# Kernel tuning notes

Measured on AMD Instinct MI355X. Metric: run time of the kernel, lower is better.

Reference implementation:

```python
import jax, jax.numpy as jnp
import numpy as np

V, D, H, L, B, S = 32000, 512, 512, 2, 64, 64
PAD = 0
NEG = -1000000000.0


def setup_inputs() -> dict:
    key = jax.random.key(0)
    ks = jax.random.split(key, 12)
    s = 0.05
    X = jax.random.randint(ks[0], (B, S), 0, V)
    enc = jax.random.normal(ks[1], (B, S - 1, H), jnp.float32)
    mask = jnp.zeros((S - 1, S - 1), dtype=bool)
    emb = jax.random.normal(ks[2], (V, D), jnp.float32) * s
    lstm_Wih = jax.random.normal(ks[3], (L, 4 * H, D), jnp.float32) * s  # D == H so stacking works for layer>0
    lstm_Whh = jax.random.normal(ks[4], (L, 4 * H, H), jnp.float32) * s
    lstm_bih = jax.random.normal(ks[5], (L, 4 * H), jnp.float32) * s
    lstm_bhh = jax.random.normal(ks[6], (L, 4 * H), jnp.float32) * s
    attn_Wh = jax.random.normal(ks[7], (H, H), jnp.float32) * s  # attn weight cols acting on decoder hidden
    attn_We = jax.random.normal(ks[8], (H, H), jnp.float32) * s  # attn weight cols acting on encoder outputs
    attn_b = jax.random.normal(ks[9], (H,), jnp.float32) * s
    v_w = jax.random.normal(ks[10], (H,), jnp.float32) * s
    fc_W = jax.random.normal(ks[11], (V, 2 * H), jnp.float32) * s
    fc_b = jnp.zeros((V,), jnp.float32)
    return {"X": X, "encoderOutputs": enc, "mask": mask, "emb": emb,
            "lstm_Wih": lstm_Wih, "lstm_Whh": lstm_Whh, "lstm_bih": lstm_bih, "lstm_bhh": lstm_bhh,
            "attn_Wh": attn_Wh, "attn_We": attn_We, "attn_b": attn_b, "v_w": v_w,
            "fc_W": fc_W, "fc_b": fc_b}


def _forward(X, enc, mask, emb, Wih, Whh, bih, bhh, attn_Wh, attn_We, attn_b, v_w, fc_W, fc_b):
    Bn, Sn = X.shape
    T = Sn - 1
    E = emb[X[:, :-1]]  # [B,T,D]
    # encoder part of attention projection is time-invariant: hoist out of the loop
    enc_proj = jnp.einsum('beh,kh->bek', enc, attn_We) + attn_b  # [B,T,H]
    h0 = jnp.zeros((L, Bn, H), E.dtype)
    c0 = jnp.zeros((L, Bn, H), E.dtype)
    xs = (jnp.transpose(E, (1, 0, 2)), X[:, 1:].T, jnp.arange(T))

    def step(carry, x_t):
        h, c = carry
        e_t, tgt, t = x_t
        inp = e_t
        hs, cs = [], []
        for l in range(L):  # fixed small layer loop
            g = inp @ Wih[l].T + h[l] @ Whh[l].T + bih[l] + bhh[l]
            i, f, gg, o = jnp.split(g, 4, axis=-1)  # torch gate order i,f,g,o
            cn = jax.nn.sigmoid(f) * c[l] + jax.nn.sigmoid(i) * jnp.tanh(gg)
            hn = jax.nn.sigmoid(o) * jnp.tanh(cn)
            hs.append(hn); cs.append(cn)
            inp = hn
        h = jnp.stack(hs); c = jnp.stack(cs)
        top = inp  # [B,H] == LSTM output of last layer
        energy = jnp.tanh((top @ attn_Wh.T)[:, None, :] + enc_proj)  # [B,T,H]
        scores = energy @ v_w  # [B,T]
        # original: self.mask[t-1] (python negative wrap) then mask.unsqueeze(0).unsqueeze(1)
        m = mask[(t - 1) % mask.shape[0], :T]  # [T]
        s3 = jnp.where(m[None, None, :], NEG, scores[None])  # broadcast -> [1,B,T]
        att = jax.nn.softmax(s3, axis=1)[0]  # softmax over batch dim, as in original
        weighted = jnp.einsum('be,beh->bh', att, enc)
        logits = jnp.concatenate([top, weighted], axis=1) @ fc_W.T + fc_b  # [B,V]
        logp = jax.nn.log_softmax(logits, axis=-1)
        nll = -jnp.take_along_axis(logp, tgt[:, None], axis=1)[:, 0]
        valid = tgt != PAD
        loss_t = jnp.sum(jnp.where(valid, nll, 0.0)) / jnp.sum(valid)  # CE mean with ignore_index
        return (h, c), loss_t

    _, losses = jax.lax.scan(step, (h0, c0), xs)
    return jnp.mean(losses)  # totalLoss / (seq_len - 1)


def reference(X, encoderOutputs, mask, emb, lstm_Wih, lstm_Whh, lstm_bih, lstm_bhh, attn_Wh, attn_We, attn_b, v_w, fc_W, fc_b):
    return _forward(X, encoderOutputs, mask, emb, lstm_Wih, lstm_Whh, lstm_bih, lstm_bhh, attn_Wh, attn_We, attn_b, v_w, fc_W, fc_b)
```

## Files before the change

### kernel.cpp

```cpp
#include <hip/hip_runtime.h>
#include <math.h>

#define NEGV -1000000000.0f

typedef unsigned short u16;
typedef __attribute__((ext_vector_type(8))) short bf16x8;
typedef __attribute__((ext_vector_type(4))) float f32x4;

__device__ __forceinline__ u16 f2bf(float f){
  union { float f; unsigned u; } v; v.f = f;
  unsigned u = v.u;
  unsigned r = (u + 0x7fffu + ((u >> 16) & 1u)) >> 16;
  return (u16)r;
}
__device__ __forceinline__ float bf2f(u16 b){
  union { unsigned u; float f; } v; v.u = ((unsigned)b) << 16;
  return v.f;
}
__device__ __forceinline__ float sigmf(float x){ return 1.f / (1.f + __expf(-x)); }
__device__ __forceinline__ float tanhf_(float x){
  float e = __expf(-2.f * fabsf(x));
  float t = (1.f - e) / (1.f + e);
  return x >= 0.f ? t : -t;
}
__device__ __forceinline__ float wred64(float v){
  #pragma unroll
  for (int m = 32; m; m >>= 1) v += __shfl_xor(v, m, 64);
  return v;
}
__device__ __forceinline__ float wmax64(float v){
  #pragma unroll
  for (int m = 32; m; m >>= 1) v = fmaxf(v, __shfl_xor(v, m, 64));
  return v;
}

typedef const __attribute__((address_space(1))) unsigned int* gas_ptr;
typedef __attribute__((address_space(3))) unsigned int* las_ptr;
__device__ __forceinline__ void gl_lds16(const u16* g, u16* l){
  __builtin_amdgcn_global_load_lds((gas_ptr)g, (las_ptr)l, 16, 0, 0);
}

__global__ __launch_bounds__(256) void k_prep(
    const float* wih, const float* whh, const float* we, const float* wh,
    const float* fcw, const float* enc, const float* bih, const float* bhh,
    u16* wihb, u16* whhb, u16* web, u16* whb, u16* fcwb, u16* encb, float* b01)
{
  const long n0 = 2097152, n1 = 2097152, n2 = 262144, n3 = 262144;
  const long n4 = 32768000, n5 = 2064384, n6 = 4096;
  const long total = n0 + n1 + n2 + n3 + n4 + n5 + n6;
  long stride = (long)gridDim.x * 256;
  for (long i = (long)blockIdx.x * 256 + threadIdx.x; i < total; i += stride){
    long j = i;
    if (j < n0){ wihb[j] = f2bf(wih[j]); continue; } j -= n0;
    if (j < n1){ whhb[j] = f2bf(whh[j]); continue; } j -= n1;
    if (j < n2){ web[j]  = f2bf(we[j]);  continue; } j -= n2;
    if (j < n3){ whb[j]  = f2bf(wh[j]);  continue; } j -= n3;
    if (j < n4){ fcwb[j] = f2bf(fcw[j]); continue; } j -= n4;
    if (j < n5){ encb[j] = f2bf(enc[j]); continue; } j -= n5;
    b01[j] = bih[j] + bhh[j];
  }
}

__global__ __launch_bounds__(256) void k_embed(const int* X, const float* emb, u16* ebf){
  int row = blockIdx.x;
  int t = row >> 6, b = row & 63;
  int tok = X[b * 64 + t];
  const float* src = emb + (long)tok * 512;
  u16* dst = ebf + (long)row * 512;
  for (int j = threadIdx.x; j < 512; j += 256) dst[j] = f2bf(src[j]);
}

__global__ __launch_bounds__(256) void gemm_bt(
    const u16* Am, int lda, const u16* Bm, int ldb,
    float* C, int ldc, const float* bias, int K)
{
  __shared__ u16 sA[64 * 32], sB[64 * 32];
  int tm = blockIdx.x, tn = blockIdx.y;
  int tid = threadIdx.x;
  int wave = tid >> 6, lane = tid & 63;
  int wm = wave >> 1, wn = wave & 1;
  int q = lane >> 4, cl = lane & 15;
  f32x4 acc[2][2];
  #pragma unroll
  for (int i = 0; i < 2; i++)
    #pragma unroll
    for (int j = 0; j < 2; j++) acc[i][j] = (f32x4){0.f, 0.f, 0.f, 0.f};

  int r = tid >> 2, ck = tid & 3;
  const u16* Ags = Am + (long)(tm * 64 + r) * lda + ck * 8;
  const u16* Bgs = Bm + (long)(tn * 64 + r) * ldb + ck * 8;
  u16* sAw = &sA[wave * 512];
  u16* sBw = &sB[wave * 512];

  for (int kt = 0; kt < K; kt += 32){
    gl_lds16(Ags + kt, sAw);
    gl_lds16(Bgs + kt, sBw);
    __syncthreads();
    #pragma unroll
    for (int i = 0; i < 2; i++){
      bf16x8 af = *(const bf16x8*)&sA[(wm * 32 + i * 16 + cl) * 32 + q * 8];
      #pragma unroll
      for (int j = 0; j < 2; j++){
        bf16x8 bfv = *(const bf16x8*)&sB[(wn * 32 + j * 16 + cl) * 32 + q * 8];
        acc[i][j] = __builtin_amdgcn_mfma_f32_16x16x32_bf16(af, bfv, acc[i][j], 0, 0, 0);
      }
    }
    __syncthreads();
  }
  #pragma unroll
  for (int i = 0; i < 2; i++)
    #pragma unroll
    for (int j = 0; j < 2; j++){
      int colg = tn * 64 + wn * 32 + j * 16 + cl;
      float bv = bias ? bias[colg] : 0.f;
      #pragma unroll
      for (int rr = 0; rr < 4; rr++){
        int rowg = tm * 64 + wm * 32 + i * 16 + q * 4 + rr;
        C[(long)rowg * ldc + colg] = acc[i][j][rr] + bv;
      }
    }
}

__global__ __launch_bounds__(256) void gemm_btb(
    const u16* Am, int lda, const u16* Bm, int ldb,
    u16* C, int ldc, const float* bias, int K)
{
  __shared__ u16 sA[64 * 32], sB[64 * 32];
  int tm = blockIdx.x, tn = blockIdx.y;
  int tid = threadIdx.x;
  int wave = tid >> 6, lane = tid & 63;
  int wm = wave >> 1, wn = wave & 1;
  int q = lane >> 4, cl = lane & 15;
  f32x4 acc[2][2];
  #pragma unroll
  for (int i = 0; i < 2; i++)
    #pragma unroll
    for (int j = 0; j < 2; j++) acc[i][j] = (f32x4){0.f, 0.f, 0.f, 0.f};

  int r = tid >> 2, ck = tid & 3;
  const u16* Ags = Am + (long)(tm * 64 + r) * lda + ck * 8;
  const u16* Bgs = Bm + (long)(tn * 64 + r) * ldb + ck * 8;
  u16* sAw = &sA[wave * 512];
  u16* sBw = &sB[wave * 512];

  for (int kt = 0; kt < K; kt += 32){
    gl_lds16(Ags + kt, sAw);
    gl_lds16(Bgs + kt, sBw);
    __syncthreads();
    #pragma unroll
    for (int i = 0; i < 2; i++){
      bf16x8 af = *(const bf16x8*)&sA[(wm * 32 + i * 16 + cl) * 32 + q * 8];
      #pragma unroll
      for (int j = 0; j < 2; j++){
        bf16x8 bfv = *(const bf16x8*)&sB[(wn * 32 + j * 16 + cl) * 32 + q * 8];
        acc[i][j] = __builtin_amdgcn_mfma_f32_16x16x32_bf16(af, bfv, acc[i][j], 0, 0, 0);
      }
    }
    __syncthreads();
  }
  #pragma unroll
  for (int i = 0; i < 2; i++)
    #pragma unroll
    for (int j = 0; j < 2; j++){
      int colg = tn * 64 + wn * 32 + j * 16 + cl;
      float bv = bias ? bias[colg] : 0.f;
      #pragma unroll
      for (int rr = 0; rr < 4; rr++){
        int rowg = tm * 64 + wm * 32 + i * 16 + q * 4 + rr;
        C[(long)rowg * ldc + colg] = f2bf(acc[i][j][rr] + bv);
      }
    }
}

__device__ __forceinline__ void wait_flags(int* flags, int tid, int need0, int need1){
  if (tid < 64){
    int need = (tid < 32) ? need0 : need1;
    for (;;){
      int v = __hip_atomic_load(flags + tid, __ATOMIC_RELAXED, __HIP_MEMORY_SCOPE_AGENT);
      if (__ballot(v >= need) == ~0ull) break;
      __builtin_amdgcn_s_sleep(1);
    }
    __builtin_amdgcn_fence(__ATOMIC_ACQUIRE, "agent");
  }
  __syncthreads();
}

__global__ __launch_bounds__(256, 1) void lstm_pipe(
    const u16* whh0, const u16* wih1, const u16* whh1,
    const u16* x0b, const float* b1s,
    u16* ring0, u16* ring1, u16* feat, int* flags)
{
  __shared__ u16 sW[32768];
  __shared__ u16 sW2[32768];
  int wg = blockIdx.x;
  int layer = wg >> 5;
  int cc = (wg & 31) * 16;
  int tid = threadIdx.x;
  int wave = tid >> 6, lane = tid & 63;
  int q = lane >> 4, cl = lane & 15;
  int j = cc + cl;

  {
    const u16* src = layer ? whh1 : whh0;
    for (int ch = tid; ch < 4096; ch += 256){
      int row = ch >> 6, c = ch & 63;
      int g = row >> 4, r = row & 15;
      *(uint4*)&sW[((c * 4 + g) * 16 + r) * 8] =
          *(const uint4*)&src[(long)(g * 512 + cc + r) * 512 + c * 8];
      if (layer)
        *(uint4*)&sW2[((c * 4 + g) * 16 + r) * 8] =
            *(const uint4*)&wih1[(long)(g * 512 + cc + r) * 512 + c * 8];
    }
  }
  __syncthreads();

  float cst[4] = {0.f, 0.f, 0.f, 0.f};
  float bg[4];
  if (layer){
    #pragma unroll
    for (int g = 0; g < 4; g++) bg[g] = b1s[g * 512 + j];
  }

  const int LOW = -(1 << 30);

  for (int t = 0; t < 63; t++){
    f32x4 acc[4];
    #pragma unroll
    for (int g = 0; g < 4; g++) acc[g] = (f32x4){0.f, 0.f, 0.f, 0.f};

    if (layer == 0){
      float xg[4][4];
      #pragma unroll
      for (int rr = 0; rr < 4; rr++){
        int s = wave * 16 + q * 4 + rr;
        const u16* xr = x0b + (long)(t * 64 + s) * 2048 + j;
        #pragma unroll
        for (int g = 0; g < 4; g++) xg[g][rr] = bf2f(xr[g * 512]);
      }
      wait_flags(flags, tid, t, t - 3);
      const u16* h0p = ring0 + ((t + 3) & 3) * 32768;
      const u16* Ab = h0p + (wave * 16 + cl) * 512 + q * 8;
      #pragma unroll
      for (int kt = 0; kt < 16; kt++){
        bf16x8 af = *(const bf16x8*)(Ab + kt * 32);
        #pragma unroll
        for (int g = 0; g < 4; g++){
          bf16x8 bfv = *(const bf16x8*)&sW[(((kt * 4 + q) * 4 + g) * 16 + cl) * 8];
          acc[g] = __builtin_amdgcn_mfma_f32_16x16x32_bf16(af, bfv, acc[g], 0, 0, 0);
        }
      }
      u16* hn = ring0 + (t & 3) * 32768;
      #pragma unroll
      for (int rr = 0; rr < 4; rr++){
        int s = wave * 16 + q * 4 + rr;
        float gi = acc[0][rr] + xg[0][rr];
        float gf = acc[1][rr] + xg[1][rr];
        float gg = acc[2][rr] + xg[2][rr];
        float go = acc[3][rr] + xg[3][rr];
        float cn = sigmf(gf) * cst[rr] + sigmf(gi) * tanhf_(gg);
        cst[rr] = cn;
        hn[s * 512 + j] = f2bf(sigmf(go) * tanhf_(cn));
      }
    } else {
      wait_flags(flags, tid, LOW, t);
      {
        const u16* h1p = ring1 + ((t + 3) & 3) * 32768;
        const u16* Ab = h1p + (wave * 16 + cl) * 512 + q * 8;
        #pragma unroll
        for (int kt = 0; kt < 16; kt++){
          bf16x8 af = *(const bf16x8*)(Ab + kt * 32);
          #pragma unroll
          for (int g = 0; g < 4; g++){
            bf16x8 bfv = *(const bf16x8*)&sW[(((kt * 4 + q) * 4 + g) * 16 + cl) * 8];
            acc[g] = __builtin_amdgcn_mfma_f32_16x16x32_bf16(af, bfv, acc[g], 0, 0, 0);
          }
        }
      }
      wait_flags(flags, tid, t + 1, LOW);
      {
        const u16* h0c = ring0 + (t & 3) * 32768;
        const u16* Ab = h0c + (wave * 16 + cl) * 512 + q * 8;
        #pragma unroll
        for (int kt = 0; kt < 16; kt++){
          bf16x8 af = *(const bf16x8*)(Ab + kt * 32);
          #pragma unroll
          for (int g = 0; g < 4; g++){
            bf16x8 bfv = *(const bf16x8*)&sW2[(((kt * 4 + q) * 4 + g) * 16 + cl) * 8];
            acc[g] = __builtin_amdgcn_mfma_f32_16x16x32_bf16(af, bfv, acc[g], 0, 0, 0);
          }
        }
      }
      u16* hn = ring1 + (t & 3) * 32768;
      #pragma unroll
      for (int rr = 0; rr < 4; rr++){
        int s = wave * 16 + q * 4 + rr;
        float gi = acc[0][rr] + bg[0];
        float gf = acc[1][rr] + bg[1];
        float gg = acc[2][rr] + bg[2];
        float go = acc[3][rr] + bg[3];
        float cn = sigmf(gf) * cst[rr] + sigmf(gi) * tanhf_(gg);
        cst[rr] = cn;
        u16 hb = f2bf(sigmf(go) * tanhf_(cn));
        hn[s * 512 + j] = hb;
        feat[(long)(t * 64 + s) * 1024 + j] = hb;
      }
    }
    __syncthreads();
    if (tid == 0)
      __hip_atomic_store(flags + wg, t + 1, __ATOMIC_RELEASE, __HIP_MEMORY_SCOPE_AGENT);
  }
}

__global__ __launch_bounds__(256) void k_scores(
    const float* qb, const float* encp, const float* vw, float* scores)
{
  int row = blockIdx.x;
  int b = row & 63;
  int wave = threadIdx.x >> 6, lane = threadIdx.x & 63;
  float qv[8], vwv[8];
  const float* qr = qb + (long)row * 512 + lane * 8;
  #pragma unroll
  for (int i = 0; i < 8; i++){ qv[i] = qr[i]; vwv[i] = vw[lane * 8 + i]; }
  for (int e = wave; e < 63; e += 4){
    const float* er = encp + (long)(b * 63 + e) * 512 + lane * 8;
    float s = 0.f;
    #pragma unroll
    for (int i = 0; i < 8; i++) s += vwv[i] * tanhf_(qv[i] + er[i]);
    s = wred64(s);
    if (lane == 0) scores[(long)row * 63 + e] = s;
  }
}

__global__ __launch_bounds__(64) void k_att(float* scores, const unsigned char* mask){
  int idx = blockIdx.x;
  int t = idx / 63, e = idx - t * 63;
  int lane = threadIdx.x;
  long off = (long)(t * 64 + lane) * 63 + e;
  float s = scores[off];
  if (mask[((t + 62) % 63) * 63 + e]) s = NEGV;
  float M = wmax64(s);
  float p = __expf(s - M);
  float S = wred64(p);
  scores[off] = p / S;
}

__global__ __launch_bounds__(256) void k_weighted(
    const float* att, const float* enc, u16* feat)
{
  int row = blockIdx.x;
  int b = row & 63;
  int j = threadIdx.x;
  float a0 = 0.f, a1 = 0.f;
  const float* ar = att + (long)row * 63;
  const float* er = enc + (long)b * 63 * 512;
  for (int e = 0; e < 63; e++){
    float a = ar[e];
    a0 += a * er[(long)e * 512 + j];
    a1 += a * er[(long)e * 512 + j + 256];
  }
  feat[(long)row * 1024 + 512 + j] = f2bf(a0);
  feat[(long)row * 1024 + 768 + j] = f2bf(a1);
}

__global__ __launch_bounds__(256) void gemm_fc(
    const u16* Am, const u16* Bm, const float* fcb, float* partials)
{
  __shared__ u16 sA[128 * 32], sB[128 * 32];
  __shared__ float sm[128][2], ss[128][2];
  int tm = blockIdx.x, tn = blockIdx.y;
  int tid = threadIdx.x;
  int wave = tid >> 6, lane = tid & 63;
  int wm = wave >> 1, wn = wave & 1;
  int q = lane >> 4, cl = lane & 15;
  f32x4 acc[4][4];
  #pragma unroll
  for (int i = 0; i < 4; i++)
    #pragma unroll
    for (int j = 0; j < 4; j++) acc[i][j] = (f32x4){0.f, 0.f, 0.f, 0.f};

  const u16 *Ag[2], *Bg[2];
  u16 *sAd[2], *sBd[2];
  #pragma unroll
  for (int h = 0; h < 2; h++){
    int idx = h * 256 + tid, rr = idx >> 2, ck = idx & 3;
    Ag[h] = Am + (long)(tm * 128 + rr) * 1024 + ck * 8;
    Bg[h] = Bm + (long)(tn * 128 + rr) * 1024 + ck * 8;
    sAd[h] = &sA[(h * 4 + wave) * 512];
    sBd[h] = &sB[(h * 4 + wave) * 512];
  }
  for (int kt = 0; kt < 1024; kt += 32){
    #pragma unroll
    for (int h = 0; h < 2; h++){
      gl_lds16(Ag[h] + kt, sAd[h]);
      gl_lds16(Bg[h] + kt, sBd[h]);
    }
    __syncthreads();
    bf16x8 afr[4];
    #pragma unroll
    for (int mt = 0; mt < 4; mt++)
      afr[mt] = *(const bf16x8*)&sA[(wm * 64 + mt * 16 + cl) * 32 + q * 8];
    #pragma unroll
    for (int nt = 0; nt < 4; nt++){
      bf16x8 bfv = *(const bf16x8*)&sB[(wn * 64 + nt * 16 + cl) * 32 + q * 8];
      #pragma unroll
      for (int mt = 0; mt < 4; mt++)
        acc[mt][nt] = __builtin_amdgcn_mfma_f32_16x16x32_bf16(afr[mt], bfv, acc[mt][nt], 0, 0, 0);
    }
    __syncthreads();
  }
  float fb[4];
  #pragma unroll
  for (int nt = 0; nt < 4; nt++) fb[nt] = fcb[tn * 128 + wn * 64 + nt * 16 + cl];
  #pragma unroll
  for (int mt = 0; mt < 4; mt++){
    #pragma unroll
    for (int rr = 0; rr < 4; rr++){
      float vals[4];
      float vm = -3.0e38f, vs = 0.f;
      #pragma unroll
      for (int nt = 0; nt < 4; nt++){ float v = acc[mt][nt][rr] + fb[nt]; vals[nt] = v; vm = fmaxf(vm, v); }
      #pragma unroll
      for (int nt = 0; nt < 4; nt++) vs += __expf(vals[nt] - vm);
      #pragma unroll
      for (int m = 1; m < 16; m <<= 1){
        float om = __shfl_xor(vm, m, 16);
        float os = __shfl_xor(vs, m, 16);
        float nm = fmaxf(vm, om);
        vs = vs * __expf(vm - nm) + os * __expf(om - nm);
        vm = nm;
      }
      if (cl == 0){ int rl = wm * 64 + mt * 16 + q * 4 + rr; sm[rl][wn] = vm; ss[rl][wn] = vs; }
    }
  }
  __syncthreads();
  if (tid < 128){
    float m0 = sm[tid][0], m1 = sm[tid][1];
    float M = fmaxf(m0, m1);
    float S = ss[tid][0] * __expf(m0 - M) + ss[tid][1] * __expf(m1 - M);
    long row = tm * 128 + tid;
    partials[(row * 250 + tn) * 2]     = M;
    partials[(row * 250 + tn) * 2 + 1] = S;
  }
}

__global__ __launch_bounds__(256) void k_rowstats(
    const float* partials, const u16* feat, const u16* fcwb,
    const float* fcb, const int* X, float* nll)
{
  int row = blockIdx.x * 4 + (threadIdx.x >> 6);
  int lane = threadIdx.x & 63;
  if (row >= 4032) return;
  float vm = -3.0e38f, vs = 0.f;
  const float* pr = partials + (long)row * 500;
  for (int i = lane; i < 250; i += 64){
    float m = pr[i * 2], s2 = pr[i * 2 + 1];
    float nm = fmaxf(vm, m);
    vs = vs * __expf(vm - nm) + s2 * __expf(m - nm);
    vm = nm;
  }
  #pragma unroll
  for (int m = 32; m; m >>= 1){
    float om = __shfl_xor(vm, m, 64);
    float os = __shfl_xor(vs, m, 64);
    float nm = fmaxf(vm, om);
    vs = vs * __expf(vm - nm) + os * __expf(om - nm);
    vm = nm;
  }
  float logZ = vm + __logf(vs);
  int t = row >> 6, b = row & 63;
  int tgt = X[b * 64 + t + 1];
  const u16* fr = feat + (long)row * 1024 + lane * 16;
  const u16* wr = fcwb + (long)tgt * 1024 + lane * 16;
  float d = 0.f;
  #pragma unroll
  for (int i = 0; i < 16; i++) d += bf2f(fr[i]) * bf2f(wr[i]);
  d = wred64(d);
  if (lane == 0) nll[row] = logZ - (d + fcb[tgt]);
}

__global__ __launch_bounds__(256) void k_final(const float* nll, const int* X, float* out){
  __shared__ float lt[64];
  int wave = threadIdx.x >> 6, lane = threadIdx.x & 63;
  for (int t = wave; t < 63; t += 4){
    int tgt = X[lane * 64 + t + 1];
    float v = (tgt != 0) ? nll[t * 64 + lane] : 0.f;
    float c = (tgt != 0) ? 1.f : 0.f;
    v = wred64(v); c = wred64(c);
    if (lane == 0) lt[t] = v / c;
  }
  __syncthreads();
  if (threadIdx.x == 0){
    float s = 0.f;
    for (int t = 0; t < 63; t++) s += lt[t];
    out[0] = s / 63.f;
  }
}

extern "C" void kernel_launch(void* const* d_in, const int* in_sizes, int n_in,
                              void* d_out, int out_size, void* d_ws, size_t ws_size,
                              hipStream_t stream)
{
  (void)in_sizes; (void)n_in; (void)out_size; (void)ws_size;
  const int*   X    = (const int*)d_in[0];
  const float* enc  = (const float*)d_in[1];
  const unsigned char* mask = (const unsigned char*)d_in[2];
  const float* emb  = (const float*)d_in[3];
  const float* wih  = (const float*)d_in[4];
  const float* whh  = (const float*)d_in[5];
  const float* bih  = (const float*)d_in[6];
  const float* bhh  = (const float*)d_in[7];
  const float* awh  = (const float*)d_in[8];
  const float* awe  = (const float*)d_in[9];
  const float* ab   = (const float*)d_in[10];
  const float* vw   = (const float*)d_in[11];
  const float* fcw  = (const float*)d_in[12];
  const float* fcb  = (const float*)d_in[13];
  float* out = (float*)d_out;

  char* w = (char*)d_ws;
  size_t o = 0;
  auto alloc = [&](size_t bytes){ size_t r = o; o = (o + bytes + 255) & ~(size_t)255; return r; };
  size_t o_ebf  = alloc((size_t)4032 * 512 * 2);
  size_t o_wihb = alloc((size_t)2 * 2048 * 512 * 2);
  size_t o_whhb = alloc((size_t)2 * 2048 * 512 * 2);
  size_t o_web  = alloc((size_t)512 * 512 * 2);
  size_t o_whb  = alloc((size_t)512 * 512 * 2);
  size_t o_fcwb = alloc((size_t)32000 * 1024 * 2);
  size_t o_encb = alloc((size_t)4032 * 512 * 2);
  size_t o_b01  = alloc((size_t)4096 * 4);
  size_t o_x0   = alloc((size_t)4032 * 2048 * 2);
  size_t o_encp = alloc((size_t)4032 * 512 * 4);
  size_t o_q    = alloc((size_t)4032 * 512 * 4);
  size_t o_feat = alloc((size_t)4096 * 1024 * 2);
  size_t o_ring = alloc((size_t)2 * 4 * 32768 * 2);
  size_t o_flags= alloc((size_t)256);
  size_t o_sc   = alloc((size_t)63 * 64 * 63 * 4);
  size_t o_part = alloc((size_t)4096 * 250 * 2 * 4);
  size_t o_nll  = alloc((size_t)4032 * 4);

  u16* ebf   = (u16*)(w + o_ebf);
  u16* wihb  = (u16*)(w + o_wihb);
  u16* whhb  = (u16*)(w + o_whhb);
  u16* web   = (u16*)(w + o_web);
  u16* whb   = (u16*)(w + o_whb);
  u16* fcwb  = (u16*)(w + o_fcwb);
  u16* encb  = (u16*)(w + o_encb);
  float* b01 = (float*)(w + o_b01);
  u16* x0b   = (u16*)(w + o_x0);
  float* encp= (float*)(w + o_encp);
  float* qb  = (float*)(w + o_q);
  u16* feat  = (u16*)(w + o_feat);
  u16* ring0 = (u16*)(w + o_ring);
  u16* ring1 = ring0 + 4 * 32768;
  int* flags = (int*)(w + o_flags);
  float* sc  = (float*)(w + o_sc);
  float* part= (float*)(w + o_part);
  float* nllb= (float*)(w + o_nll);

  hipMemsetAsync(w + o_ring, 0, (o_flags - o_ring) + 256, stream);

  k_prep<<<4096, 256, 0, stream>>>(wih, whh, awe, awh, fcw, enc, bih, bhh,
                                   wihb, whhb, web, whb, fcwb, encb, b01);
  k_embed<<<4032, 256, 0, stream>>>(X, emb, ebf);

  gemm_btb<<<dim3(63, 32), 256, 0, stream>>>(ebf, 512, wihb, 512, x0b, 2048, b01, 512);
  gemm_bt<<<dim3(63, 8), 256, 0, stream>>>(encb, 512, web, 512, encp, 512, ab, 512);

  lstm_pipe<<<64, 256, 0, stream>>>(whhb, wihb + 2048 * 512, whhb + 2048 * 512,
                                    x0b, b01 + 2048, ring0, ring1, feat, flags);

  gemm_bt<<<dim3(63, 8), 256, 0, stream>>>(feat, 1024, whb, 512, qb, 512, nullptr, 512);
  k_scores<<<4032, 256, 0, stream>>>(qb, encp, vw, sc);
  k_att<<<3969, 64, 0, stream>>>(sc, mask);
  k_weighted<<<4032, 256, 0, stream>>>(sc, enc, feat);

  gemm_fc<<<dim3(32, 250), 256, 0, stream>>>(feat, fcwb, fcb, part);
  k_rowstats<<<1008, 256, 0, stream>>>(part, feat, fcwb, fcb, X, nllb);
  k_final<<<1, 256, 0, stream>>>(nllb, X, out);
}
```

Measured before the change: 1.501 ms.

## Replace acquire/release fences with sc1 loads/stores in LSTM pipeline handoff

The persistent LSTM pipeline now writes hidden states to the ring buffers with sc1 stores and reads them back with batched sc1 dwordx4 loads. This lets it drop the agent-scope acquire fence and release ordering on the flag handshake. The spin-wait sleep is also removed and all 16 A fragments are loaded up front before the MFMA loop. The aim is to cut per-timestep cross-workgroup synchronisation latency (cache invalidate/writeback fences) on the serial recurrence. The risk is memory-ordering correctness, which now depends on the sc1 cache-coherence semantics, and busy spinning adds memory traffic.

```diff
diff --git a/kernel.cpp b/kernel.cpp
--- a/kernel.cpp
+++ b/kernel.cpp
@@ -38,6 +38,10 @@
 typedef __attribute__((address_space(3))) unsigned int* las_ptr;
 __device__ __forceinline__ void gl_lds16(const u16* g, u16* l){
   __builtin_amdgcn_global_load_lds((gas_ptr)g, (las_ptr)l, 16, 0, 0);
+}
+
+__device__ __forceinline__ void st_sc1_u16(u16* p, unsigned v){
+  asm volatile("global_store_short %0, %1, off sc1" :: "v"(p), "v"(v) : "memory");
 }
 
 __global__ __launch_bounds__(256) void k_prep(
@@ -178,12 +182,20 @@
     for (;;){
       int v = __hip_atomic_load(flags + tid, __ATOMIC_RELAXED, __HIP_MEMORY_SCOPE_AGENT);
       if (__ballot(v >= need) == ~0ull) break;
-      __builtin_amdgcn_s_sleep(1);
-    }
-    __builtin_amdgcn_fence(__ATOMIC_ACQUIRE, "agent");
+    }
   }
   __syncthreads();
 }
+
+#define LOAD_RING_FRAGS(afr, Ab)                                              \
+  {                                                                            \
+    _Pragma("unroll")                                                          \
+    for (int kt = 0; kt < 16; kt++)                                            \
+      asm volatile("global_load_dwordx4 %0, %1, off offset:%2 sc1"             \
+                   : "=v"(afr[kt]) : "v"(Ab), "i"(kt * 64));                   \
+    asm volatile("s_waitcnt vmcnt(0)" ::: "memory");                           \
+    __builtin_amdgcn_sched_barrier(0);                                         \
+  }
 
 __global__ __launch_bounds__(256, 1) void lstm_pipe(
     const u16* whh0, const u16* wih1, const u16* whh1,
@@ -238,16 +250,17 @@
         for (int g = 0; g < 4; g++) xg[g][rr] = bf2f(xr[g * 512]);
       }
       wait_flags(flags, tid, t, t - 3);
-      const u16* h0p = ring0 + ((t + 3) & 3) * 32768;
-      const u16* Ab = h0p + (wave * 16 + cl) * 512 + q * 8;
-      #pragma unroll
-      for (int kt = 0; kt < 16; kt++){
-        bf16x8 af = *(const bf16x8*)(Ab + kt * 32);
+      {
+        const u16* Ab = ring0 + ((t + 3) & 3) * 32768 + (wave * 16 + cl) * 512 + q * 8;
+        bf16x8 afr[16];
+        LOAD_RING_FRAGS(afr, Ab);
         #pragma unroll
-        for (int g = 0; g < 4; g++){
-          bf16x8 bfv = *(const bf16x8*)&sW[(((kt * 4 + q) * 4 + g) * 16 + cl) * 8];
-          acc[g] = __builtin_amdgcn_mfma_f32_16x16x32_bf16(af, bfv, acc[g], 0, 0, 0);
-        }
+        for (int kt = 0; kt < 16; kt++)
+          #pragma unroll
+          for (int g = 0; g < 4; g++){
+            bf16x8 bfv = *(const bf16x8*)&sW[(((kt * 4 + q) * 4 + g) * 16 + cl) * 8];
+            acc[g] = __builtin_amdgcn_mfma_f32_16x16x32_bf16(afr[kt], bfv, acc[g], 0, 0, 0);
+          }
       }
       u16* hn = ring0 + (t & 3) * 32768;
       #pragma unroll
@@ -259,36 +272,34 @@
         float go = acc[3][rr] + xg[3][rr];
         float cn = sigmf(gf) * cst[rr] + sigmf(gi) * tanhf_(gg);
         cst[rr] = cn;
-        hn[s * 512 + j] = f2bf(sigmf(go) * tanhf_(cn));
+        st_sc1_u16(hn + s * 512 + j, (unsigned)f2bf(sigmf(go) * tanhf_(cn)));
       }
     } else {
       wait_flags(flags, tid, LOW, t);
       {
-        const u16* h1p = ring1 + ((t + 3) & 3) * 32768;
-        const u16* Ab = h1p + (wave * 16 + cl) * 512 + q * 8;
+        const u16* Ab = ring1 + ((t + 3) & 3) * 32768 + (wave * 16 + cl) * 512 + q * 8;
+        bf16x8 afr[16];
+        LOAD_RING_FRAGS(afr, Ab);
         #pragma unroll
-        for (int kt = 0; kt < 16; kt++){
-          bf16x8 af = *(const bf16x8*)(Ab + kt * 32);
+        for (int kt = 0; kt < 16; kt++)
           #pragma unroll
           for (int g = 0; g < 4; g++){
             bf16x8 bfv = *(const bf16x8*)&sW[(((kt * 4 + q) * 4 + g) * 16 + cl) * 8];
-            acc[g] = __builtin_amdgcn_mfma_f32_16x16x32_bf16(af, bfv, acc[g], 0, 0, 0);
+            acc[g] = __builtin_amdgcn_mfma_f32_16x16x32_bf16(afr[kt], bfv, acc[g], 0, 0, 0);
           }
-        }
       }
       wait_flags(flags, tid, t + 1, LOW);
       {
-        const u16* h0c = ring0 + (t & 3) * 32768;
-        const u16* Ab = h0c + (wave * 16 + cl) * 512 + q * 8;
+        const u16* Ab = ring0 + (t & 3) * 32768 + (wave * 16 + cl) * 512 + q * 8;
+        bf16x8 afr[16];
+        LOAD_RING_FRAGS(afr, Ab);
         #pragma unroll
-        for (int kt = 0; kt < 16; kt++){
-          bf16x8 af = *(const bf16x8*)(Ab + kt * 32);
+        for (int kt = 0; kt < 16; kt++)
           #pragma unroll
           for (int g = 0; g < 4; g++){
             bf16x8 bfv = *(const bf16x8*)&sW2[(((kt * 4 + q) * 4 + g) * 16 + cl) * 8];
-            acc[g] = __builtin_amdgcn_mfma_f32_16x16x32_bf16(af, bfv, acc[g], 0, 0, 0);
+            acc[g] = __builtin_amdgcn_mfma_f32_16x16x32_bf16(afr[kt], bfv, acc[g], 0, 0, 0);
           }
-        }
       }
       u16* hn = ring1 + (t & 3) * 32768;
       #pragma unroll
@@ -301,13 +312,14 @@
         float cn = sigmf(gf) * cst[rr] + sigmf(gi) * tanhf_(gg);
         cst[rr] = cn;
         u16 hb = f2bf(sigmf(go) * tanhf_(cn));
-        hn[s * 512 + j] = hb;
+        st_sc1_u16(hn + s * 512 + j, (unsigned)hb);
         feat[(long)(t * 64 + s) * 1024 + j] = hb;
       }
     }
+    asm volatile("s_waitcnt vmcnt(0)" ::: "memory");
     __syncthreads();
     if (tid == 0)
-      __hip_atomic_store(flags + wg, t + 1, __ATOMIC_RELEASE, __HIP_MEMORY_SCOPE_AGENT);
+      __hip_atomic_store(flags + wg, t + 1, __ATOMIC_RELAXED, __HIP_MEMORY_SCOPE_AGENT);
   }
 }
 
```

Result: faster. 1.363 ms (-9.2%).
